# Kernel tuning notes

Hardware: AMD Instinct MI355X
Metric: run time of the kernel (lower is better)

## Reference

```python
import jax, jax.numpy as jnp
import numpy as np

TOP_K = 3
COMMIT = 0.25


def setup_inputs() -> dict:
    key = jax.random.key(0)
    k1, k2, k3 = jax.random.split(key, 3)
    features = jax.random.normal(k1, (197, 128, 768), dtype=jnp.float32)
    class_emb = jax.random.normal(k2, (4096, 768), dtype=jnp.float32)
    feat_emb = jax.random.normal(k3, (4096, 768), dtype=jnp.float32)
    return {"features": features, "class_emb": class_emb, "feat_emb": feat_emb}


def _vq(x, emb):
    # x: [A, B, C]; emb: [K, C]
    A, B, C = x.shape
    K = emb.shape[0]
    N = A * B
    flat = x.reshape(N, C)
    d = (jnp.sum(flat * flat, axis=1, keepdims=True)
         + jnp.sum(emb * emb, axis=1)
         - 2.0 * flat @ emb.T)                      # [N, K]
    _, idx = jax.lax.top_k(-d, TOP_K)               # smallest-k indices [N, k]
    quant = emb[idx].reshape(A, B, TOP_K, C)        # gather codewords
    xr = x[:, :, None, :]                           # [A, B, 1, C]
    e_latent_loss = jnp.mean((jax.lax.stop_gradient(quant) - jnp.broadcast_to(xr, quant.shape)) ** 2)
    loss = COMMIT * e_latent_loss
    q_st = xr + jax.lax.stop_gradient(quant - xr)   # straight-through [A,B,k,C]
    # avg_probs: mean over rows of the top-k one-hot encodings (rows sum to k)
    counts = jnp.zeros((K,), x.dtype).at[idx.reshape(-1)].add(1.0)
    avg_probs = counts / N
    perplexity = jnp.exp(-jnp.sum(avg_probs * jnp.log(avg_probs + 1e-10)))
    return loss, q_st, perplexity, avg_probs, idx.reshape(A, B, TOP_K), d.reshape(A, B, K)


def _forward(features, class_emb, feat_emb):
    cl_loss, cl_q, cl_perp, cl_avg, cl_idx, cl_dist = _vq(features[0:1], class_emb)
    ft_loss, ft_q, ft_perp, ft_avg, ft_idx, ft_dist = _vq(features[1:], feat_emb)
    Kc = class_emb.shape[0]
    Kf = feat_emb.shape[0]
    FMAX = jnp.float32(np.finfo(np.float32).max)
    B = features.shape[1]
    T = features.shape[0] - 1
    cl_dist_p = jnp.concatenate([cl_dist, jnp.full((1, B, Kf), FMAX, jnp.float32)], axis=-1)
    ft_dist_p = jnp.concatenate([jnp.full((T, B, Kc), FMAX, jnp.float32), ft_dist], axis=-1)
    distances = jnp.concatenate([cl_dist_p, ft_dist_p], axis=0)          # [T+1, B, Kc+Kf]
    encoding_indices = jnp.concatenate([cl_idx, ft_idx + Kc], axis=0)    # [T+1, B, k]
    quantized = jnp.concatenate([cl_q, ft_q], axis=0)                    # [T+1, B, k, C]
    loss = ft_loss + cl_loss
    return (loss, quantized, cl_perp, ft_perp, cl_avg, ft_avg, encoding_indices, distances)


def reference(features, class_emb, feat_emb):
    return _forward(features, class_emb, feat_emb)
```

## Files before the change

kernel.cpp:

```cpp
#include <hip/hip_runtime.h>
#include <math.h>

#define DEVFN __device__ __forceinline__

typedef short  s16x8 __attribute__((ext_vector_type(8)));
typedef float  f32x4 __attribute__((ext_vector_type(4)));

constexpr int C     = 768;
constexpr int NROWS = 25216;
constexpr int NCL   = 128;
constexpr int KCB   = 4096;
constexpr int KOUT  = 8192;
constexpr int TK    = 3;
constexpr int NT    = 24;
constexpr int MT    = 197;
constexpr int NTL   = 32;

constexpr long long QUANT_OFF  = 1;
constexpr long long QUANT_SZ   = (long long)NROWS * TK * C;
constexpr long long CLPERP_OFF = QUANT_OFF + QUANT_SZ;
constexpr long long FTPERP_OFF = CLPERP_OFF + 1;
constexpr long long CLAVG_OFF  = FTPERP_OFF + 1;
constexpr long long FTAVG_OFF  = CLAVG_OFF + KCB;
constexpr long long ENC_OFF    = FTAVG_OFF + KCB;
constexpr long long DIST_OFF   = ENC_OFF + (long long)NROWS * TK;

constexpr size_t XS_ELE = (size_t)MT * NT * 4096;
constexpr size_t ES_ELE = (size_t)2 * NTL * NT * 4096;

constexpr float FMAXV = 3.4028234663852886e38f;
constexpr float PADV  = 3.3895313892515355e38f;

DEVFN void gload_lds16(const void* g, void* l) {
    __builtin_amdgcn_global_load_lds(
        (const __attribute__((address_space(1))) unsigned*)g,
        (__attribute__((address_space(3))) unsigned*)l, 16, 0, 0);
}

DEVFN bool better(float v, int i, float bv, int bi) {
    return (v < bv) | ((v == bv) & (i < bi));
}
DEVFN void ins3(float v, int i, float& v0, int& i0, float& v1, int& i1, float& v2, int& i2) {
    const bool b0 = better(v, i, v0, i0);
    const bool b1 = better(v, i, v1, i1);
    const bool b2 = better(v, i, v2, i2);
    const float nv1 = b0 ? v0 : (b1 ? v : v1);
    const int   ni1 = b0 ? i0 : (b1 ? i : i1);
    const float nv2 = b1 ? v1 : (b2 ? v : v2);
    const int   ni2 = b1 ? i1 : (b2 ? i : i2);
    v0 = b0 ? v : v0;  i0 = b0 ? i : i0;
    v1 = nv1;          i1 = ni1;
    v2 = nv2;          i2 = ni2;
}

__global__ void init_kernel(float* counts) {
    int i = blockIdx.x * blockDim.x + threadIdx.x;
    if (i < KOUT) counts[i] = 0.0f;
}

__global__ void norms_kernel(const float* __restrict__ X,
                             const float* __restrict__ CE,
                             const float* __restrict__ FE,
                             float* __restrict__ xnorm,
                             float* __restrict__ enorm) {
    int row  = blockIdx.x * 4 + (threadIdx.x >> 6);
    int lane = threadIdx.x & 63;
    const int TOT = NROWS + 2 * KCB;
    if (row >= TOT) return;
    const float* src; float* dst;
    if (row < NROWS) { src = X + (long long)row * C; dst = xnorm + row; }
    else {
        int r = row - NROWS;
        src = (r < KCB) ? (CE + (long long)r * C) : (FE + (long long)(r - KCB) * C);
        dst = enorm + r;
    }
    const float4* p = (const float4*)src;
    float s = 0.f;
    for (int j = lane; j < C / 4; j += 64) {
        float4 v = p[j];
        s += v.x*v.x + v.y*v.y + v.z*v.z + v.w*v.w;
    }
    for (int o = 32; o > 0; o >>= 1) s += __shfl_down(s, o);
    if (lane == 0) *dst = s;
}

__global__ __launch_bounds__(256)
void presplit_kernel(const float* __restrict__ X,
                     const float* __restrict__ CE,
                     const float* __restrict__ FE,
                     short* __restrict__ XsH, short* __restrict__ XsL,
                     short* __restrict__ EsH, short* __restrict__ EsL) {
    const int b = blockIdx.x;
    const float* src; char* dH; char* dL;
    if (b < MT * NT) {
        const int tile = b / NT, ks = b % NT;
        src = X + (size_t)tile * 128 * C + ks * 32;
        dH = (char*)(XsH + (size_t)b * 4096);
        dL = (char*)(XsL + (size_t)b * 4096);
    } else {
        const int bb = b - MT * NT;
        const int book = bb / (NTL * NT);
        const int rem  = bb % (NTL * NT);
        const int tile = rem / NT, ks = rem % NT;
        src = (book ? FE : CE) + (size_t)tile * 128 * C + ks * 32;
        dH = (char*)(EsH + (size_t)bb * 4096);
        dL = (char*)(EsL + (size_t)bb * 4096);
    }
    const int tid = threadIdx.x;
    const int row = tid >> 2, oc = tid & 3;
    #pragma unroll
    for (int rr = 0; rr < 2; ++rr) {
        const int r = row + rr * 64;
        const float* s = src + (size_t)r * C + oc * 8;
        float4 v0 = *(const float4*)s;
        float4 v1 = *(const float4*)(s + 4);
        float f[8] = {v0.x, v0.y, v0.z, v0.w, v1.x, v1.y, v1.z, v1.w};
        s16x8 hi, lo;
        #pragma unroll
        for (int q = 0; q < 8; ++q) {
            unsigned u = __float_as_uint(f[q]);
            hi[q] = (short)(u >> 16);
            lo[q] = (short)(__float_as_uint(f[q] - __uint_as_float(u & 0xffff0000u)) >> 16);
        }
        const int off = (r * 64 + oc * 16) ^ ((r & 7) << 4);
        *(s16x8*)(dH + off) = hi;
        *(s16x8*)(dL + off) = lo;
    }
}

__global__ __launch_bounds__(256)
void gemm_dist_kernel(const short* __restrict__ XsH, const short* __restrict__ XsL,
                      const short* __restrict__ EsH, const short* __restrict__ EsL,
                      const float* __restrict__ xnorm,
                      const float* __restrict__ enorm,
                      float* __restrict__ dist) {
    __shared__ __align__(16) char smem[2 * 4 * 8192];

    const int orig = blockIdx.y * gridDim.x + blockIdx.x;
    const int wg   = (orig & 7) * 788 + (orig >> 3);
    const int mt = wg >> 5, nt = wg & 31;

    const int m0 = mt * 128, n0 = nt * 128;
    const int colbase = (mt == 0) ? 0 : KCB;
    const int btile = ((mt == 0) ? 0 : NTL) + nt;
    const int tid = threadIdx.x, l = tid & 63, w = tid >> 6;
    const int wy = w >> 1, wx = w & 1;

    const char* gsrc[4] = {
        (const char*)XsH + (size_t)mt * NT * 8192,
        (const char*)XsL + (size_t)mt * NT * 8192,
        (const char*)EsH + (size_t)btile * NT * 8192,
        (const char*)EsL + (size_t)btile * NT * 8192
    };

    const int arow = wy * 64 + (l & 15);
    const int brow = wx * 64 + (l & 15);
    const int abase = (arow * 64 + ((l >> 4) * 16)) ^ ((l & 7) << 4);
    const int bbase = (brow * 64 + ((l >> 4) * 16)) ^ ((l & 7) << 4);

    auto STAGE = [&](int buf, int t) {
        const size_t tb = (size_t)t * 8192;
        #pragma unroll
        for (int p = 0; p < 4; ++p)
            #pragma unroll
            for (int i = 0; i < 2; ++i) {
                const int chunk = w * 2 + i;
                gload_lds16(gsrc[p] + tb + chunk * 1024 + l * 16,
                            smem + buf * 32768 + p * 8192 + chunk * 1024);
            }
    };

    f32x4 acc[4][4];
    #pragma unroll
    for (int i = 0; i < 4; ++i)
        #pragma unroll
        for (int j = 0; j < 4; ++j) acc[i][j] = (f32x4){0.f, 0.f, 0.f, 0.f};

    STAGE(0, 0);
    asm volatile("s_waitcnt vmcnt(0)" ::: "memory");
    __syncthreads();

    int cur = 0;
    for (int t = 0; t < NT; ++t) {
        if (t + 1 < NT) STAGE(cur ^ 1, t + 1);

        const char* sb = smem + cur * 32768;
        s16x8 ah[4], bh[4];
        #pragma unroll
        for (int i = 0; i < 4; ++i) ah[i] = *(const s16x8*)(sb + abase + i * 1024);
        #pragma unroll
        for (int j = 0; j < 4; ++j) bh[j] = *(const s16x8*)(sb + 16384 + bbase + j * 1024);
        #pragma unroll
        for (int i = 0; i < 4; ++i)
            #pragma unroll
            for (int j = 0; j < 4; ++j)
                acc[i][j] = __builtin_amdgcn_mfma_f32_16x16x32_bf16(ah[i], bh[j], acc[i][j], 0, 0, 0);

        s16x8 al[4];
        #pragma unroll
        for (int i = 0; i < 4; ++i) al[i] = *(const s16x8*)(sb + 8192 + abase + i * 1024);
        #pragma unroll
        for (int i = 0; i < 4; ++i)
            #pragma unroll
            for (int j = 0; j < 4; ++j)
                acc[i][j] = __builtin_amdgcn_mfma_f32_16x16x32_bf16(al[i], bh[j], acc[i][j], 0, 0, 0);

        s16x8 bl[4];
        #pragma unroll
        for (int j = 0; j < 4; ++j) bl[j] = *(const s16x8*)(sb + 24576 + bbase + j * 1024);
        #pragma unroll
        for (int i = 0; i < 4; ++i)
            #pragma unroll
            for (int j = 0; j < 4; ++j)
                acc[i][j] = __builtin_amdgcn_mfma_f32_16x16x32_bf16(ah[i], bl[j], acc[i][j], 0, 0, 0);

        if (t + 1 < NT) {
            asm volatile("s_waitcnt vmcnt(0)" ::: "memory");
            __syncthreads();
            cur ^= 1;
        }
    }

    const int lr = (l >> 4) * 4;
    const int lc = l & 15;
    float en_r[4];
    #pragma unroll
    for (int j = 0; j < 4; ++j) en_r[j] = enorm[colbase + n0 + wx * 64 + j * 16 + lc];
    #pragma unroll
    for (int i = 0; i < 4; ++i) {
        #pragma unroll
        for (int q = 0; q < 4; ++q) {
            const int gm = m0 + wy * 64 + i * 16 + lr + q;
            const float xnv = xnorm[gm];
            float* o = dist + (long long)gm * KOUT + colbase + n0 + wx * 64 + lc;
            #pragma unroll
            for (int j = 0; j < 4; ++j)
                o[j * 16] = (xnv + en_r[j]) - 2.0f * acc[i][j][q];
        }
    }

    const int padbase = (mt == 0) ? KCB : 0;
    for (int r2 = w; r2 < 128; r2 += 4) {
        float* p = dist + (long long)(m0 + r2) * KOUT + padbase + n0;
        p[l] = PADV; p[l + 64] = PADV;
    }
}

__global__ __launch_bounds__(256)
void topk_kernel(const float* __restrict__ dist,
                 int* __restrict__ idxbuf,
                 float* __restrict__ out,
                 float* __restrict__ counts) {
    int rb = blockIdx.x * 4 + (threadIdx.x >> 6);
    if (rb >= NROWS) return;
    const int row = NROWS - 1 - rb;
    const int lane = threadIdx.x & 63;
    const int colbase = (row < NCL) ? 0 : KCB;
    const float* d = dist + (long long)row * KOUT + colbase;
    float v0 = FMAXV, v1 = FMAXV, v2 = FMAXV;
    int   i0 = 0x7fffffff, i1 = 0x7fffffff, i2 = 0x7fffffff;

    const float4* dv = (const float4*)(d + 1);

    float4 b[8];
    #pragma unroll
    for (int it = 0; it < 8; ++it) b[it] = dv[it * 64 + lane];
    #pragma unroll
    for (int it = 0; it < 8; ++it) {
        const int k = 1 + (it * 64 + lane) * 4;
        ins3(b[it].x, k,     v0, i0, v1, i1, v2, i2);
        ins3(b[it].y, k + 1, v0, i0, v1, i1, v2, i2);
        ins3(b[it].z, k + 2, v0, i0, v1, i1, v2, i2);
        ins3(b[it].w, k + 3, v0, i0, v1, i1, v2, i2);
    }
    #pragma unroll
    for (int it = 0; it < 7; ++it) b[it] = dv[(8 + it) * 64 + lane];
    const bool hasLast = (960 + lane) < 1023;
    b[7] = hasLast ? dv[960 + lane]
                   : (float4){FMAXV, FMAXV, FMAXV, FMAXV};
    #pragma unroll
    for (int it = 0; it < 7; ++it) {
        const int k = 1 + ((8 + it) * 64 + lane) * 4;
        ins3(b[it].x, k,     v0, i0, v1, i1, v2, i2);
        ins3(b[it].y, k + 1, v0, i0, v1, i1, v2, i2);
        ins3(b[it].z, k + 2, v0, i0, v1, i1, v2, i2);
        ins3(b[it].w, k + 3, v0, i0, v1, i1, v2, i2);
    }
    {
        const int k = 1 + (960 + lane) * 4;
        const int kk = hasLast ? k : 0x7ffffff0;
        ins3(b[7].x, kk,     v0, i0, v1, i1, v2, i2);
        ins3(b[7].y, kk + 1, v0, i0, v1, i1, v2, i2);
        ins3(b[7].z, kk + 2, v0, i0, v1, i1, v2, i2);
        ins3(b[7].w, kk + 3, v0, i0, v1, i1, v2, i2);
    }
    if (lane < 4) {
        const int k = (lane == 0) ? 0 : 4092 + lane;
        ins3(d[k], k, v0, i0, v1, i1, v2, i2);
    }

    #pragma unroll
    for (int off = 32; off > 0; off >>= 1) {
        float w0 = __shfl_down(v0, off), w1 = __shfl_down(v1, off), w2 = __shfl_down(v2, off);
        int   j0 = __shfl_down(i0, off), j1 = __shfl_down(i1, off), j2 = __shfl_down(i2, off);
        ins3(w0, j0, v0, i0, v1, i1, v2, i2);
        ins3(w1, j1, v0, i0, v1, i1, v2, i2);
        ins3(w2, j2, v0, i0, v1, i1, v2, i2);
    }
    if (lane == 0) {
        long long rt = (long long)row * TK;
        idxbuf[rt + 0] = i0; idxbuf[rt + 1] = i1; idxbuf[rt + 2] = i2;
        out[ENC_OFF + rt + 0] = (float)(i0 + colbase);
        out[ENC_OFF + rt + 1] = (float)(i1 + colbase);
        out[ENC_OFF + rt + 2] = (float)(i2 + colbase);
        atomicAdd(&counts[i0 + colbase], 1.0f);
        atomicAdd(&counts[i1 + colbase], 1.0f);
        atomicAdd(&counts[i2 + colbase], 1.0f);
    }
}

__global__ __launch_bounds__(192)
void gather_kernel(const float* __restrict__ X,
                   const float* __restrict__ CE,
                   const float* __restrict__ FE,
                   const int* __restrict__ idxbuf,
                   float* __restrict__ out,
                   float* __restrict__ partials) {
    const int row = blockIdx.x;
    const int tid = threadIdx.x;
    const float4 xv = ((const float4*)(X + (size_t)row * C))[tid];
    const float* Ebase = (row < NCL) ? CE : FE;
    const long long rt0 = (long long)row * TK;
    float s = 0.f;
    #pragma unroll
    for (int t = 0; t < TK; ++t) {
        const int id = idxbuf[rt0 + t];
        const float4 ev = ((const float4*)(Ebase + (size_t)id * C))[tid];
        const float d0 = ev.x - xv.x, d1 = ev.y - xv.y, d2 = ev.z - xv.z, d3 = ev.w - xv.w;
        s += d0*d0 + d1*d1 + d2*d2 + d3*d3;
        float* q = out + QUANT_OFF + (rt0 + t) * C + tid * 4;
        q[0] = xv.x + d0; q[1] = xv.y + d1; q[2] = xv.z + d2; q[3] = xv.w + d3;
    }
    #pragma unroll
    for (int o = 32; o > 0; o >>= 1) s += __shfl_down(s, o);
    __shared__ float red[3];
    const int lane = tid & 63, w = tid >> 6;
    if (lane == 0) red[w] = s;
    __syncthreads();
    if (tid == 0) partials[row] = red[0] + red[1] + red[2];
}

__global__ void finalize_kernel(const float* __restrict__ counts,
                                const float* __restrict__ partials,
                                float* __restrict__ out) {
    __shared__ float  red[2][4];
    __shared__ double redd[2][4];
    int tid = threadIdx.x, lane = tid & 63, w = tid >> 6;
    float ecl = 0.f, eft = 0.f;
    for (int i = tid; i < KCB; i += blockDim.x) {
        float p = counts[i] * (1.0f / 128.0f);
        out[CLAVG_OFF + i] = p;
        ecl += p * logf(p + 1e-10f);
        float qv = counts[KCB + i] * (1.0f / 25088.0f);
        out[FTAVG_OFF + i] = qv;
        eft += qv * logf(qv + 1e-10f);
    }
    double scl = 0.0, sft = 0.0;
    for (int i = tid; i < NROWS; i += blockDim.x) {
        double v = (double)partials[i];
        if (i < NCL) scl += v; else sft += v;
    }
    for (int o = 32; o > 0; o >>= 1) {
        ecl += __shfl_down(ecl, o); eft += __shfl_down(eft, o);
        scl += __shfl_down(scl, o); sft += __shfl_down(sft, o);
    }
    if (lane == 0) { red[0][w] = ecl; red[1][w] = eft; redd[0][w] = scl; redd[1][w] = sft; }
    __syncthreads();
    if (tid == 0) {
        float tcl = red[0][0] + red[0][1] + red[0][2] + red[0][3];
        float tft = red[1][0] + red[1][1] + red[1][2] + red[1][3];
        double dcl = redd[0][0] + redd[0][1] + redd[0][2] + redd[0][3];
        double dft = redd[1][0] + redd[1][1] + redd[1][2] + redd[1][3];
        out[CLPERP_OFF] = expf(-tcl);
        out[FTPERP_OFF] = expf(-tft);
        float cl_loss = 0.25f * (float)(dcl / 294912.0);
        float ft_loss = 0.25f * (float)(dft / 57802752.0);
        out[0] = ft_loss + cl_loss;
    }
}

extern "C" void kernel_launch(void* const* d_in, const int* in_sizes, int n_in,
                              void* d_out, int out_size, void* d_ws, size_t ws_size,
                              hipStream_t stream) {
    const float* X  = (const float*)d_in[0];
    const float* CE = (const float*)d_in[1];
    const float* FE = (const float*)d_in[2];
    float* out = (float*)d_out;

    float* ws_f   = (float*)d_ws;
    float* xnorm  = ws_f;
    float* enorm  = ws_f + NROWS;
    float* counts = ws_f + NROWS + KOUT;
    int*   idxbuf = (int*)(ws_f + NROWS + 2 * KOUT);
    float* ssepart = xnorm;
    float* dist   = out + DIST_OFF;

    short* XsH = (short*)(out + 4);
    short* XsL = XsH + XS_ELE;
    short* EsH = XsL + XS_ELE;
    short* EsL = EsH + ES_ELE;

    init_kernel<<<32, 256, 0, stream>>>(counts);
    norms_kernel<<<(NROWS + 2 * KCB) / 4, 256, 0, stream>>>(X, CE, FE, xnorm, enorm);
    presplit_kernel<<<MT * NT + 2 * NTL * NT, 256, 0, stream>>>(X, CE, FE, XsH, XsL, EsH, EsL);
    gemm_dist_kernel<<<dim3(NTL, MT), 256, 0, stream>>>(XsH, XsL, EsH, EsL, xnorm, enorm, dist);
    topk_kernel<<<NROWS / 4, 256, 0, stream>>>(dist, idxbuf, out, counts);
    gather_kernel<<<NROWS, 192, 0, stream>>>(X, CE, FE, idxbuf, out, ssepart);
    finalize_kernel<<<1, 256, 0, stream>>>(counts, ssepart, out);
}
```

Before: 1.759 ms.

## Widen GEMM tile to 128x256 with 8 waves and split-waitcnt pipelining

The distance GEMM tile grows from 128x128 to 128x256 columns. Each block now runs 512 threads (8 waves in a 2x4 grid), and the codebook pre-split is regrouped into 256-row tiles to match. The double-buffered prefetch now waits with vmcnt(6), so the next stage's loads stay in flight while the current tile is consumed, and raw s_barrier plus sched_barrier fences replace __syncthreads. The aim is more reuse of each loaded X tile and better overlap of loads with MFMA work, at the cost of 96KB of LDS per block and only two blocks per CU.

```diff
diff --git a/kernel.cpp b/kernel.cpp
--- a/kernel.cpp
+++ b/kernel.cpp
@@ -14,7 +14,7 @@
 constexpr int TK    = 3;
 constexpr int NT    = 24;
 constexpr int MT    = 197;
-constexpr int NTL   = 32;
+constexpr int NTB   = 16;
 
 constexpr long long QUANT_OFF  = 1;
 constexpr long long QUANT_SZ   = (long long)NROWS * TK * C;
@@ -26,7 +26,7 @@
 constexpr long long DIST_OFF   = ENC_OFF + (long long)NROWS * TK;
 
 constexpr size_t XS_ELE = (size_t)MT * NT * 4096;
-constexpr size_t ES_ELE = (size_t)2 * NTL * NT * 4096;
+constexpr size_t ES_ELE = (size_t)2 * NTB * NT * 8192;
 
 constexpr float FMAXV = 3.4028234663852886e38f;
 constexpr float PADV  = 3.3895313892515355e38f;
@@ -91,25 +91,26 @@
                      short* __restrict__ XsH, short* __restrict__ XsL,
                      short* __restrict__ EsH, short* __restrict__ EsL) {
     const int b = blockIdx.x;
-    const float* src; char* dH; char* dL;
+    const float* src; char* dH; char* dL; int nrr;
     if (b < MT * NT) {
         const int tile = b / NT, ks = b % NT;
         src = X + (size_t)tile * 128 * C + ks * 32;
         dH = (char*)(XsH + (size_t)b * 4096);
         dL = (char*)(XsL + (size_t)b * 4096);
+        nrr = 2;
     } else {
         const int bb = b - MT * NT;
-        const int book = bb / (NTL * NT);
-        const int rem  = bb % (NTL * NT);
+        const int book = bb / (NTB * NT);
+        const int rem  = bb % (NTB * NT);
         const int tile = rem / NT, ks = rem % NT;
-        src = (book ? FE : CE) + (size_t)tile * 128 * C + ks * 32;
-        dH = (char*)(EsH + (size_t)bb * 4096);
-        dL = (char*)(EsL + (size_t)bb * 4096);
+        src = (book ? FE : CE) + (size_t)tile * 256 * C + ks * 32;
+        dH = (char*)(EsH + (size_t)bb * 8192);
+        dL = (char*)(EsL + (size_t)bb * 8192);
+        nrr = 4;
     }
     const int tid = threadIdx.x;
     const int row = tid >> 2, oc = tid & 3;
-    #pragma unroll
-    for (int rr = 0; rr < 2; ++rr) {
+    for (int rr = 0; rr < nrr; ++rr) {
         const int r = row + rr * 64;
         const float* s = src + (size_t)r * C + oc * 8;
         float4 v0 = *(const float4*)s;
@@ -128,29 +129,41 @@
     }
 }
 
-__global__ __launch_bounds__(256)
+__global__ __launch_bounds__(512, 2)
 void gemm_dist_kernel(const short* __restrict__ XsH, const short* __restrict__ XsL,
                       const short* __restrict__ EsH, const short* __restrict__ EsL,
                       const float* __restrict__ xnorm,
                       const float* __restrict__ enorm,
                       float* __restrict__ dist) {
-    __shared__ __align__(16) char smem[2 * 4 * 8192];
+    __shared__ __align__(16) char smem[2 * 49152];
 
     const int orig = blockIdx.y * gridDim.x + blockIdx.x;
-    const int wg   = (orig & 7) * 788 + (orig >> 3);
-    const int mt = wg >> 5, nt = wg & 31;
-
-    const int m0 = mt * 128, n0 = nt * 128;
+    const int wg   = (orig & 7) * 394 + (orig >> 3);
+    const int mt = wg >> 4, nt = wg & 15;
+
+    const int m0 = mt * 128, n0 = nt * 256;
     const int colbase = (mt == 0) ? 0 : KCB;
-    const int btile = ((mt == 0) ? 0 : NTL) + nt;
+    const int btile = ((mt == 0) ? 0 : NTB) + nt;
     const int tid = threadIdx.x, l = tid & 63, w = tid >> 6;
-    const int wy = w >> 1, wx = w & 1;
-
-    const char* gsrc[4] = {
-        (const char*)XsH + (size_t)mt * NT * 8192,
-        (const char*)XsL + (size_t)mt * NT * 8192,
-        (const char*)EsH + (size_t)btile * NT * 8192,
-        (const char*)EsL + (size_t)btile * NT * 8192
+    const int wy = w >> 2, wx = w & 3;
+
+    const char* sbase[6]; size_t sstr[6]; int ldso[6];
+    #pragma unroll
+    for (int i = 0; i < 6; ++i) {
+        const int wc = w * 6 + i;
+        const char* pb; int within; size_t st;
+        if (wc < 8)       { pb = (const char*)XsH + (size_t)mt * NT * 8192;     within = wc * 1024;        st = 8192;  }
+        else if (wc < 16) { pb = (const char*)XsL + (size_t)mt * NT * 8192;     within = (wc - 8) * 1024;  st = 8192;  }
+        else if (wc < 32) { pb = (const char*)EsH + (size_t)btile * NT * 16384; within = (wc - 16) * 1024; st = 16384; }
+        else              { pb = (const char*)EsL + (size_t)btile * NT * 16384; within = (wc - 32) * 1024; st = 16384; }
+        sbase[i] = pb + within + l * 16;
+        sstr[i]  = st;
+        ldso[i]  = wc * 1024 + l * 16;
+    }
+    auto STAGE = [&](int buf, int t) {
+        #pragma unroll
+        for (int i = 0; i < 6; ++i)
+            gload_lds16(sbase[i] + (size_t)t * sstr[i], smem + buf * 49152 + ldso[i]);
     };
 
     const int arow = wy * 64 + (l & 15);
@@ -158,18 +171,6 @@
     const int abase = (arow * 64 + ((l >> 4) * 16)) ^ ((l & 7) << 4);
     const int bbase = (brow * 64 + ((l >> 4) * 16)) ^ ((l & 7) << 4);
 
-    auto STAGE = [&](int buf, int t) {
-        const size_t tb = (size_t)t * 8192;
-        #pragma unroll
-        for (int p = 0; p < 4; ++p)
-            #pragma unroll
-            for (int i = 0; i < 2; ++i) {
-                const int chunk = w * 2 + i;
-                gload_lds16(gsrc[p] + tb + chunk * 1024 + l * 16,
-                            smem + buf * 32768 + p * 8192 + chunk * 1024);
-            }
-    };
-
     f32x4 acc[4][4];
     #pragma unroll
     for (int i = 0; i < 4; ++i)
@@ -177,14 +178,18 @@
         for (int j = 0; j < 4; ++j) acc[i][j] = (f32x4){0.f, 0.f, 0.f, 0.f};
 
     STAGE(0, 0);
-    asm volatile("s_waitcnt vmcnt(0)" ::: "memory");
-    __syncthreads();
-
     int cur = 0;
     for (int t = 0; t < NT; ++t) {
-        if (t + 1 < NT) STAGE(cur ^ 1, t + 1);
-
-        const char* sb = smem + cur * 32768;
+        if (t + 1 < NT) {
+            STAGE(cur ^ 1, t + 1);
+            asm volatile("s_waitcnt vmcnt(6)" ::: "memory");
+        } else {
+            asm volatile("s_waitcnt vmcnt(0)" ::: "memory");
+        }
+        __builtin_amdgcn_s_barrier();
+        __builtin_amdgcn_sched_barrier(0);
+
+        const char* sb = smem + cur * 49152;
         s16x8 ah[4], bh[4];
         #pragma unroll
         for (int i = 0; i < 4; ++i) ah[i] = *(const s16x8*)(sb + abase + i * 1024);
@@ -207,18 +212,17 @@
 
         s16x8 bl[4];
         #pragma unroll
-        for (int j = 0; j < 4; ++j) bl[j] = *(const s16x8*)(sb + 24576 + bbase + j * 1024);
+        for (int j = 0; j < 4; ++j) bl[j] = *(const s16x8*)(sb + 32768 + bbase + j * 1024);
         #pragma unroll
         for (int i = 0; i < 4; ++i)
             #pragma unroll
             for (int j = 0; j < 4; ++j)
                 acc[i][j] = __builtin_amdgcn_mfma_f32_16x16x32_bf16(ah[i], bl[j], acc[i][j], 0, 0, 0);
 
-        if (t + 1 < NT) {
-            asm volatile("s_waitcnt vmcnt(0)" ::: "memory");
-            __syncthreads();
-            cur ^= 1;
-        }
+        __builtin_amdgcn_sched_barrier(0);
+        asm volatile("s_waitcnt lgkmcnt(0)" ::: "memory");
+        __builtin_amdgcn_s_barrier();
+        cur ^= 1;
     }
 
     const int lr = (l >> 4) * 4;
@@ -240,9 +244,9 @@
     }
 
     const int padbase = (mt == 0) ? KCB : 0;
-    for (int r2 = w; r2 < 128; r2 += 4) {
+    for (int r2 = w; r2 < 128; r2 += 8) {
         float* p = dist + (long long)(m0 + r2) * KOUT + padbase + n0;
-        p[l] = PADV; p[l + 64] = PADV;
+        p[l] = PADV; p[l + 64] = PADV; p[l + 128] = PADV; p[l + 192] = PADV;
     }
 }
 
@@ -412,8 +416,8 @@
 
     init_kernel<<<32, 256, 0, stream>>>(counts);
     norms_kernel<<<(NROWS + 2 * KCB) / 4, 256, 0, stream>>>(X, CE, FE, xnorm, enorm);
-    presplit_kernel<<<MT * NT + 2 * NTL * NT, 256, 0, stream>>>(X, CE, FE, XsH, XsL, EsH, EsL);
-    gemm_dist_kernel<<<dim3(NTL, MT), 256, 0, stream>>>(XsH, XsL, EsH, EsL, xnorm, enorm, dist);
+    presplit_kernel<<<MT * NT + 2 * NTB * NT, 256, 0, stream>>>(X, CE, FE, XsH, XsL, EsH, EsL);
+    gemm_dist_kernel<<<dim3(NTB, MT), 512, 0, stream>>>(XsH, XsL, EsH, EsL, xnorm, enorm, dist);
     topk_kernel<<<NROWS / 4, 256, 0, stream>>>(dist, idxbuf, out, counts);
     gather_kernel<<<NROWS, 192, 0, stream>>>(X, CE, FE, idxbuf, out, ssepart);
     finalize_kernel<<<1, 256, 0, stream>>>(counts, ssepart, out);
```

Result: no change. 1.771 ms (+0.7%).
